# Kernel tuning notes

Measured on AMD Instinct MI355X. Metric: run time of the kernel, lower is better.

The kernel has to match this reference:

```python
import jax, jax.numpy as jnp
import numpy as np

N_HEADS = 16
POOL_WIDTH = 3


def setup_inputs() -> dict:
    key = jax.random.key(0)
    ks = jax.random.split(key, 6)
    B, S, D = 4, 1024, 1024
    x = jax.random.normal(ks[0], (B, S, D), dtype=jnp.float32)
    W_q = jax.random.normal(ks[1], (D, D), dtype=jnp.float32) * 0.02
    W_k = jax.random.normal(ks[2], (D, D), dtype=jnp.float32) * 0.02
    W_v = jax.random.normal(ks[3], (D, D), dtype=jnp.float32) * 0.02
    W_o = jax.random.normal(ks[4], (D, D), dtype=jnp.float32) * 0.02
    freq_raw = jnp.zeros((D,), dtype=jnp.float32)
    pool_raw = jnp.array([0.25, 1.0, 0.25], dtype=jnp.float32)
    return {"x": x, "W_q": W_q, "W_k": W_k, "W_v": W_v, "W_o": W_o,
            "freq_raw": freq_raw, "pool_raw": pool_raw}


def _spectral_attention(x, W_q, W_k, W_v, W_o, freq_raw, pool_raw):
    B, S, D = x.shape
    H = N_HEADS
    hd = D // H
    pw = POOL_WIDTH
    pad = pw // 2

    # projections (torch Linear: y = x @ W.T)
    Q = x @ W_q.T
    K = x @ W_k.T
    V = x @ W_v.T

    # monotone non-increasing freq weights: reverse cumsum of softplus
    fw = jnp.flip(jnp.cumsum(jnp.flip(jax.nn.softplus(freq_raw))))
    # symmetric, positive pool weights
    pwts = jax.nn.softplus((pool_raw + jnp.flip(pool_raw)) * 0.5)

    Qh = (Q * fw).reshape(B, S, H, hd).transpose(0, 2, 1, 3)  # [B,H,S,hd]
    K_pad = jnp.pad(K, ((0, 0), (0, 0), (pad, pad)))          # [B,S,D+2*pad]

    scores = jnp.zeros((B, H, S, S), dtype=x.dtype)
    for i in range(pw):  # small fixed loop over pool offsets
        K_shift = jax.lax.dynamic_slice_in_dim(K_pad, i, D, axis=2)
        Kh = K_shift.reshape(B, S, H, hd).transpose(0, 2, 1, 3)
        scores = scores + pwts[i] * jnp.einsum('bhqd,bhkd->bhqk', Qh, Kh)
    scores = scores / np.sqrt(hd).astype(x.dtype)

    causal = jnp.tril(jnp.ones((S, S), dtype=bool))
    scores = jnp.where(causal, scores, jnp.finfo(scores.dtype).min)
    attn = jax.nn.softmax(scores, axis=-1)

    Vh = V.reshape(B, S, H, hd).transpose(0, 2, 1, 3)
    out = jnp.einsum('bhqk,bhkd->bhqd', attn, Vh)
    out = out.transpose(0, 2, 1, 3).reshape(B, S, D)
    return out @ W_o.T


def reference(x, W_q, W_k, W_v, W_o, freq_raw, pool_raw):
    return _spectral_attention(x, W_q, W_k, W_v, W_o, freq_raw, pool_raw)
```

## Files before the change

kernel.cpp:

```cpp
#include <hip/hip_runtime.h>

typedef __attribute__((ext_vector_type(8))) short short8;
typedef __attribute__((ext_vector_type(4))) float float4v;
typedef __attribute__((ext_vector_type(4))) float floatx4;
typedef __attribute__((ext_vector_type(4))) unsigned short ushort4v;

#define DEV static __device__ __forceinline__
#define MFMA __builtin_amdgcn_mfma_f32_16x16x32_bf16

DEV unsigned short f2bf(float f){
  unsigned u = __builtin_bit_cast(unsigned, f);
  unsigned r = u + 0x7FFFu + ((u >> 16) & 1u);
  return (unsigned short)(r >> 16);
}
DEV float bf2f(unsigned short h){
  unsigned u = ((unsigned)h) << 16;
  return __builtin_bit_cast(float, u);
}
DEV float softplus_f(float x){
  if (x > 20.f) return x;
  return log1pf(expf(x));
}

DEV void gload16(const void* g, void* l){
  __builtin_amdgcn_global_load_lds(
      (const __attribute__((address_space(1))) unsigned int*)g,
      (__attribute__((address_space(3))) unsigned int*)l, 16, 0, 0);
}

__global__ void k_prep_fw(const float* __restrict__ freq_raw,
                          const float* __restrict__ pool_raw,
                          float* __restrict__ fw, float* __restrict__ pw){
  __shared__ float s[1024];
  int d = threadIdx.x;
  s[d] = softplus_f(freq_raw[d]);
  __syncthreads();
  for (int off = 1; off < 1024; off <<= 1){
    float t = (d + off < 1024) ? s[d + off] : 0.f;
    __syncthreads();
    s[d] += t;
    __syncthreads();
  }
  fw[d] = s[d];
  if (d < 3) pw[d] = softplus_f((pool_raw[d] + pool_raw[2 - d]) * 0.5f);
}

__global__ __launch_bounds__(256) void k_prep_w(
    const float* __restrict__ Wq, const float* __restrict__ Wk,
    const float* __restrict__ Wv, const float* __restrict__ Wo,
    const float* __restrict__ fw, const float* __restrict__ pw,
    unsigned short* __restrict__ wq_h, unsigned short* __restrict__ wq_l,
    unsigned short* __restrict__ wk_h, unsigned short* __restrict__ wk_l,
    unsigned short* __restrict__ wv_b, unsigned short* __restrict__ wo_b){
  int idx = blockIdx.x * 256 + threadIdx.x;
  int n  = idx >> 8;
  int k4 = (idx & 255) << 2;
  float p0 = pw[0], p1 = pw[1], p2 = pw[2];
  float f = fw[n] * 0.125f;
  int o = n * 1024 + k4;
  float4v q4 = *(const float4v*)(Wq + o);
  float4v k0v = *(const float4v*)(Wk + o);
  float4v km = {0.f,0.f,0.f,0.f}, kp = {0.f,0.f,0.f,0.f};
  if (n > 0)    km = *(const float4v*)(Wk + o - 1024);
  if (n < 1023) kp = *(const float4v*)(Wk + o + 1024);
  float4v v4 = *(const float4v*)(Wv + o);
  float4v o4 = *(const float4v*)(Wo + o);
  ushort4v qh, ql, kh, kl, vb, ob;
  for (int j = 0; j < 4; j++){
    float wq_ = f * q4[j];
    unsigned short h = f2bf(wq_);
    qh[j] = h; ql[j] = f2bf(wq_ - bf2f(h));
    float wk_ = p0 * km[j] + p1 * k0v[j] + p2 * kp[j];
    h = f2bf(wk_);
    kh[j] = h; kl[j] = f2bf(wk_ - bf2f(h));
    vb[j] = f2bf(v4[j]);
    ob[j] = f2bf(o4[j]);
  }
  *(ushort4v*)(wq_h + o) = qh; *(ushort4v*)(wq_l + o) = ql;
  *(ushort4v*)(wk_h + o) = kh; *(ushort4v*)(wk_l + o) = kl;
  *(ushort4v*)(wv_b + o) = vb; *(ushort4v*)(wo_b + o) = ob;
}

__global__ __launch_bounds__(256) void k_split_x(const float* __restrict__ x,
                                                 unsigned short* __restrict__ xh,
                                                 unsigned short* __restrict__ xl){
  int idx = blockIdx.x * 256 + threadIdx.x;
  int o = idx * 4;
  float4v v = *(const float4v*)(x + o);
  ushort4v h4, l4;
  for (int j = 0; j < 4; j++){
    unsigned short h = f2bf(v[j]);
    h4[j] = h; l4[j] = f2bf(v[j] - bf2f(h));
  }
  *(ushort4v*)(xh + o) = h4;
  *(ushort4v*)(xl + o) = l4;
}

__global__ __launch_bounds__(256) void k_gemm_qk(
    const unsigned short* __restrict__ Ah, const unsigned short* __restrict__ Al,
    const unsigned short* __restrict__ Bqh, const unsigned short* __restrict__ Bql,
    const unsigned short* __restrict__ Bkh, const unsigned short* __restrict__ Bkl,
    unsigned short* __restrict__ qh_o, unsigned short* __restrict__ ql_o,
    unsigned short* __restrict__ kh_o, unsigned short* __restrict__ kl_o){
  __shared__ unsigned short lds[2][16384];
  int tid = threadIdx.x;
  int w = tid >> 6, l = tid & 63, lg = l >> 4, lr = l & 15;
  int wr = w >> 1, wc = w & 1;
  int g = blockIdx.x;
  int mblk = (g & 7) * 4 + ((g >> 3) & 3);
  int nblk = g >> 5;
  int m0 = mblk * 128, n0 = nblk * 64;

  auto stage = [&](int kt, int bufi){
    unsigned short* buf = lds[bufi];
    for (int rep = 0; rep < 2; rep++){
      int idx = rep * 256 + tid;
      int r = idx >> 2, c = idx & 3;
      int cs = (c ^ ((r >> 1) & 3)) * 8;
      int srcA = (m0 + r) * 1024 + kt + cs;
      unsigned short* dst = buf + rep * 2048 + w * 512;
      gload16(Ah + srcA, dst);
      gload16(Al + srcA, dst + 4096);
    }
    {
      int r = tid >> 2, c = tid & 3;
      int cs = (c ^ ((r >> 1) & 3)) * 8;
      int srcB = (n0 + r) * 1024 + kt + cs;
      unsigned short* dst = buf + 8192 + w * 512;
      gload16(Bqh + srcB, dst);
      gload16(Bql + srcB, dst + 2048);
      gload16(Bkh + srcB, dst + 4096);
      gload16(Bkl + srcB, dst + 6144);
    }
  };

  floatx4 aq[4][2] = {}, ak[4][2] = {};
  stage(0, 0);
  __syncthreads();
  int cur = 0;
  for (int kt = 0; kt < 1024; kt += 32){
    if (kt + 32 < 1024) stage(kt + 32, cur ^ 1);
    const unsigned short* buf = lds[cur];
    short8 a_h[4], a_l[4], bq_h[2], bq_l[2], bk_h[2], bk_l[2];
    for (int ms = 0; ms < 4; ms++){
      int r = wr * 64 + ms * 16 + lr;
      int off = r * 32 + ((lg ^ ((r >> 1) & 3)) * 8);
      a_h[ms] = *(const short8*)(buf + off);
      a_l[ms] = *(const short8*)(buf + 4096 + off);
    }
    for (int ns = 0; ns < 2; ns++){
      int r = wc * 32 + ns * 16 + lr;
      int off = r * 32 + ((lg ^ ((r >> 1) & 3)) * 8);
      bq_h[ns] = *(const short8*)(buf + 8192 + off);
      bq_l[ns] = *(const short8*)(buf + 10240 + off);
      bk_h[ns] = *(const short8*)(buf + 12288 + off);
      bk_l[ns] = *(const short8*)(buf + 14336 + off);
    }
    for (int ms = 0; ms < 4; ms++)
      for (int ns = 0; ns < 2; ns++){
        aq[ms][ns] = MFMA(a_h[ms], bq_h[ns], aq[ms][ns], 0, 0, 0);
        aq[ms][ns] = MFMA(a_h[ms], bq_l[ns], aq[ms][ns], 0, 0, 0);
        aq[ms][ns] = MFMA(a_l[ms], bq_h[ns], aq[ms][ns], 0, 0, 0);
        ak[ms][ns] = MFMA(a_h[ms], bk_h[ns], ak[ms][ns], 0, 0, 0);
        ak[ms][ns] = MFMA(a_h[ms], bk_l[ns], ak[ms][ns], 0, 0, 0);
        ak[ms][ns] = MFMA(a_l[ms], bk_h[ns], ak[ms][ns], 0, 0, 0);
      }
    __syncthreads();
    cur ^= 1;
  }
  for (int ms = 0; ms < 4; ms++)
    for (int ns = 0; ns < 2; ns++){
      int mrow = m0 + wr * 64 + ms * 16 + lg * 4;
      int ncol = n0 + wc * 32 + ns * 16 + lr;
      for (int rr = 0; rr < 4; rr++){
        int o = (mrow + rr) * 1024 + ncol;
        float v = aq[ms][ns][rr];
        unsigned short hh = f2bf(v);
        qh_o[o] = hh; ql_o[o] = f2bf(v - bf2f(hh));
        v = ak[ms][ns][rr];
        hh = f2bf(v);
        kh_o[o] = hh; kl_o[o] = f2bf(v - bf2f(hh));
      }
    }
}

template<int OUT>
__global__ __launch_bounds__(256) void k_gemm(
    const unsigned short* __restrict__ Ah, const unsigned short* __restrict__ Bh,
    void* __restrict__ out0, int M, int N, int K){
  constexpr int BUFN = 6144;
  __shared__ unsigned short lds[2 * BUFN];
  int tid = threadIdx.x;
  int w = tid >> 6, l = tid & 63, lg = l >> 4, lr = l & 15;
  int wr = w >> 1, wc = w & 1;
  int n0 = blockIdx.x * 128, m0 = blockIdx.y * 64;

  auto stage = [&](int kt, int bufi){
    unsigned short* buf = lds + bufi * BUFN;
    { int r = tid >> 2, c = tid & 3;
      int src = (m0 + r) * K + kt + (c ^ ((r >> 1) & 3)) * 8;
      gload16(Ah + src, buf + w * 512); }
    for (int rep = 0; rep < 2; rep++){
      int idx = rep * 256 + tid;
      int r = idx >> 2, c = idx & 3;
      int src = (n0 + r) * K + kt + (c ^ ((r >> 1) & 3)) * 8;
      gload16(Bh + src, buf + 2048 + rep * 2048 + w * 512);
    }
  };

  floatx4 acc[2][4] = {};
  stage(0, 0);
  __syncthreads();
  int cur = 0;
  for (int kt = 0; kt < K; kt += 32){
    if (kt + 32 < K) stage(kt + 32, cur ^ 1);
    const unsigned short* buf = lds + cur * BUFN;
    short8 a_h[2], b_h[4];
    for (int ms = 0; ms < 2; ms++){
      int r = wr * 32 + ms * 16 + lr;
      int off = r * 32 + ((lg ^ ((r >> 1) & 3)) * 8);
      a_h[ms] = *(const short8*)(buf + off);
    }
    for (int ns = 0; ns < 4; ns++){
      int r = wc * 64 + ns * 16 + lr;
      int off = r * 32 + ((lg ^ ((r >> 1) & 3)) * 8);
      b_h[ns] = *(const short8*)(buf + 2048 + off);
    }
    for (int ms = 0; ms < 2; ms++)
      for (int ns = 0; ns < 4; ns++)
        acc[ms][ns] = MFMA(a_h[ms], b_h[ns], acc[ms][ns], 0, 0, 0);
    __syncthreads();
    cur ^= 1;
  }
  for (int ms = 0; ms < 2; ms++)
    for (int ns = 0; ns < 4; ns++){
      int mrow = m0 + wr * 32 + ms * 16 + lg * 4;
      int ncol;
      if constexpr (OUT == 3){
        int p = ((ns >> 1) << 5) | ((lr >> 2) << 3) | ((ns & 1) << 2) | (lr & 3);
        ncol = n0 + wc * 64 + p;
      } else {
        ncol = n0 + wc * 64 + ns * 16 + lr;
      }
      for (int rr = 0; rr < 4; rr++){
        float v = acc[ms][ns][rr];
        int o = (mrow + rr) * N + ncol;
        if constexpr (OUT == 2) ((float*)out0)[o] = v;
        else                    ((unsigned short*)out0)[o] = f2bf(v);
      }
    }
}

__global__ __launch_bounds__(256) void k_attn(
    const unsigned short* __restrict__ Qh, const unsigned short* __restrict__ Ql,
    const unsigned short* __restrict__ Kh, const unsigned short* __restrict__ Kl,
    const unsigned short* __restrict__ Vt, unsigned short* __restrict__ Ob){
  __shared__ unsigned short s_k[2][12288];
  int tid = threadIdx.x;
  int w = tid >> 6, l = tid & 63, lg = l >> 4, lr = l & 15;
  int gx = blockIdx.x;
  int bh = gx & 63, qt = gx >> 6;
  int b = bh >> 4, h = bh & 15;
  int q0 = qt * 64;
  int qs = q0 + w * 16;
  int rowb = b * 1024;

  auto stage = [&](int kt, int bufi){
    int k0 = kt * 64;
    unsigned short* buf = s_k[bufi];
    for (int rep = 0; rep < 2; rep++){
      int idx = rep * 256 + tid;
      int r = idx >> 3, c = idx & 7;
      int cs = c ^ (r & 7);
      int srcK = (rowb + k0 + r) * 1024 + h * 64 + cs * 8;
      int srcV = ((h * 64 + r) * 4 + b) * 1024 + k0 + cs * 8;
      unsigned short* dst = buf + rep * 2048 + w * 512;
      gload16(Kh + srcK, dst);
      gload16(Kl + srcK, dst + 4096);
      gload16(Vt + srcV, dst + 8192);
    }
  };

  short8 fqh[2], fql[2];
  for (int ds = 0; ds < 2; ds++){
    int off = (rowb + qs + lr) * 1024 + h * 64 + ds * 32 + lg * 8;
    fqh[ds] = *(const short8*)(Qh + off);
    fql[ds] = *(const short8*)(Ql + off);
  }

  floatx4 oT[4] = {};
  float m_r = -__builtin_inff(), l_r = 0.f;

  int ntile = qt + 1;
  stage(0, 0);
  __syncthreads();
  int cur = 0;
  for (int kt = 0; kt < ntile; kt++){
    int k0 = kt * 64;
    if (kt + 1 < ntile) stage(kt + 1, cur ^ 1);
    const unsigned short* kb = s_k[cur];

    floatx4 sc[4] = {};
    __builtin_amdgcn_s_setprio(1);
    for (int ds = 0; ds < 2; ds++)
      for (int s = 0; s < 4; s++){
        int r = s * 16 + lr;
        int off = r * 64 + (((ds * 4 + lg) ^ (r & 7)) * 8);
        short8 kh_f = *(const short8*)(kb + off);
        short8 kl_f = *(const short8*)(kb + 4096 + off);
        sc[s] = MFMA(kh_f, fqh[ds], sc[s], 0, 0, 0);
        sc[s] = MFMA(kl_f, fqh[ds], sc[s], 0, 0, 0);
        sc[s] = MFMA(kh_f, fql[ds], sc[s], 0, 0, 0);
      }
    __builtin_amdgcn_s_setprio(0);

    if (kt == ntile - 1){
      #pragma unroll
      for (int s = 0; s < 4; s++)
        #pragma unroll
        for (int rr = 0; rr < 4; rr++)
          if (k0 + s * 16 + 4 * lg + rr > qs + lr) sc[s][rr] = -__builtin_inff();
    }

    float mx = sc[0][0];
    #pragma unroll
    for (int s = 0; s < 4; s++)
      #pragma unroll
      for (int rr = 0; rr < 4; rr++) mx = fmaxf(mx, sc[s][rr]);
    mx = fmaxf(mx, __shfl_xor(mx, 16));
    mx = fmaxf(mx, __shfl_xor(mx, 32));
    float mn = fmaxf(m_r, mx);
    float fac = __expf(m_r - mn);
    m_r = mn;
    float ps = 0.f;
    #pragma unroll
    for (int s = 0; s < 4; s++)
      #pragma unroll
      for (int rr = 0; rr < 4; rr++){
        float p = __expf(sc[s][rr] - mn);
        sc[s][rr] = p;
        ps += p;
      }
    ps += __shfl_xor(ps, 16);
    ps += __shfl_xor(ps, 32);
    l_r = l_r * fac + ps;
    #pragma unroll
    for (int dsb = 0; dsb < 4; dsb++) oT[dsb] *= fac;

    __builtin_amdgcn_s_setprio(1);
    #pragma unroll
    for (int kk = 0; kk < 2; kk++){
      short8 pb;
      #pragma unroll
      for (int j = 0; j < 8; j++)
        pb[j] = (short)f2bf(sc[2 * kk + (j >> 2)][j & 3]);
      #pragma unroll
      for (int dsb = 0; dsb < 4; dsb++){
        int rv = dsb * 16 + lr;
        int offv = rv * 64 + (((kk * 4 + lg) ^ (rv & 7)) * 8);
        short8 vb = *(const short8*)(kb + 8192 + offv);
        oT[dsb] = MFMA(vb, pb, oT[dsb], 0, 0, 0);
      }
    }
    __builtin_amdgcn_s_setprio(0);
    __syncthreads();
    cur ^= 1;
  }

  float inv = 1.f / l_r;
  int base = (rowb + qs + lr) * 1024 + h * 64;
  #pragma unroll
  for (int dsb = 0; dsb < 4; dsb++){
    ushort4v o4;
    #pragma unroll
    for (int rr = 0; rr < 4; rr++) o4[rr] = f2bf(oT[dsb][rr] * inv);
    *(ushort4v*)(Ob + base + dsb * 16 + 4 * lg) = o4;
  }
}

extern "C" void kernel_launch(void* const* d_in, const int* in_sizes, int n_in,
                              void* d_out, int out_size, void* d_ws, size_t ws_size,
                              hipStream_t stream){
  const float* x  = (const float*)d_in[0];
  const float* Wq = (const float*)d_in[1];
  const float* Wk = (const float*)d_in[2];
  const float* Wv = (const float*)d_in[3];
  const float* Wo = (const float*)d_in[4];
  const float* fr = (const float*)d_in[5];
  const float* pr = (const float*)d_in[6];

  char* ws = (char*)d_ws;
  size_t off = 0;
  auto alloc = [&](size_t bytes) -> char* {
    char* p = ws + off;
    off += (bytes + 255) & ~(size_t)255;
    return p;
  };
  float* fw = (float*)alloc(1024 * sizeof(float));
  float* pw = (float*)alloc(256);
  const size_t WB = (size_t)1024 * 1024 * 2;
  unsigned short* wq_h = (unsigned short*)alloc(WB);
  unsigned short* wq_l = (unsigned short*)alloc(WB);
  unsigned short* wk_h = (unsigned short*)alloc(WB);
  unsigned short* wk_l = (unsigned short*)alloc(WB);
  unsigned short* wv_b = (unsigned short*)alloc(WB);
  unsigned short* wo_b = (unsigned short*)alloc(WB);
  const size_t XB = (size_t)4096 * 1024 * 2;
  unsigned short* x_h = (unsigned short*)alloc(XB);
  unsigned short* x_l = (unsigned short*)alloc(XB);
  unsigned short* q_h = (unsigned short*)alloc(XB);
  unsigned short* q_l = (unsigned short*)alloc(XB);
  unsigned short* k_h = (unsigned short*)alloc(XB);
  unsigned short* k_l = (unsigned short*)alloc(XB);
  unsigned short* vt  = (unsigned short*)alloc(XB);
  unsigned short* o_b = x_l;

  k_prep_fw<<<1, 1024, 0, stream>>>(fr, pr, fw, pw);
  k_prep_w<<<1024, 256, 0, stream>>>(Wq, Wk, Wv, Wo, fw, pw,
                                     wq_h, wq_l, wk_h, wk_l, wv_b, wo_b);
  k_split_x<<<4096, 256, 0, stream>>>(x, x_h, x_l);

  k_gemm_qk<<<512, 256, 0, stream>>>(x_h, x_l, wq_h, wq_l, wk_h, wk_l,
                                     q_h, q_l, k_h, k_l);
  dim3 ggv(32, 16);
  k_gemm<3><<<ggv, 256, 0, stream>>>(wv_b, x_h, (void*)vt, 1024, 4096, 1024);
  k_attn<<<1024, 256, 0, stream>>>(q_h, q_l, k_h, k_l, vt, o_b);
  dim3 ggo(8, 64);
  k_gemm<2><<<ggo, 256, 0, stream>>>(o_b, wo_b, d_out, 4096, 1024, 1024);
}
```

Baseline: 144.8 us.

## Triple-buffer GEMM pipelines with vmcnt waits and widen QK GEMM to 512 threads

Both GEMM kernels move from double to triple buffering in LDS, prefetching two k-tiles ahead. A partial s_waitcnt vmcnt followed by a single s_barrier per iteration replaces the two __syncthreads calls. The QK projection kernel now runs 512 threads (8 waves), each wave owning a 64x16 tile, and the MFMA order is regrouped so independent accumulators interleave. This aims to hide global load latency and raise MFMA occupancy, at the cost of more LDS per block and reliance on exact vmcnt counting of async loads.

```diff
diff --git a/kernel.cpp b/kernel.cpp
--- a/kernel.cpp
+++ b/kernel.cpp
@@ -96,92 +96,99 @@
   *(ushort4v*)(xl + o) = l4;
 }
 
-__global__ __launch_bounds__(256) void k_gemm_qk(
+__global__ __launch_bounds__(512) void k_gemm_qk(
     const unsigned short* __restrict__ Ah, const unsigned short* __restrict__ Al,
     const unsigned short* __restrict__ Bqh, const unsigned short* __restrict__ Bql,
     const unsigned short* __restrict__ Bkh, const unsigned short* __restrict__ Bkl,
     unsigned short* __restrict__ qh_o, unsigned short* __restrict__ ql_o,
     unsigned short* __restrict__ kh_o, unsigned short* __restrict__ kl_o){
-  __shared__ unsigned short lds[2][16384];
+  __shared__ unsigned short lds[3][16384];
   int tid = threadIdx.x;
   int w = tid >> 6, l = tid & 63, lg = l >> 4, lr = l & 15;
-  int wr = w >> 1, wc = w & 1;
+  int wr = w >> 2, wc = w & 3;
   int g = blockIdx.x;
   int mblk = (g & 7) * 4 + ((g >> 3) & 3);
   int nblk = g >> 5;
   int m0 = mblk * 128, n0 = nblk * 64;
 
+  const unsigned short* Bp0 = (w < 4) ? Bqh : Bql;
+  const unsigned short* Bp1 = (w < 4) ? Bkh : Bkl;
+
   auto stage = [&](int kt, int bufi){
     unsigned short* buf = lds[bufi];
-    for (int rep = 0; rep < 2; rep++){
-      int idx = rep * 256 + tid;
-      int r = idx >> 2, c = idx & 3;
-      int cs = (c ^ ((r >> 1) & 3)) * 8;
-      int srcA = (m0 + r) * 1024 + kt + cs;
-      unsigned short* dst = buf + rep * 2048 + w * 512;
-      gload16(Ah + srcA, dst);
-      gload16(Al + srcA, dst + 4096);
-    }
     {
       int r = tid >> 2, c = tid & 3;
       int cs = (c ^ ((r >> 1) & 3)) * 8;
+      int srcA = (m0 + r) * 1024 + kt + cs;
+      gload16(Ah + srcA, buf + w * 512);
+      gload16(Al + srcA, buf + 4096 + w * 512);
+    }
+    {
+      int within = tid & 255;
+      int r = within >> 2, c = within & 3;
+      int cs = (c ^ ((r >> 1) & 3)) * 8;
       int srcB = (n0 + r) * 1024 + kt + cs;
-      unsigned short* dst = buf + 8192 + w * 512;
-      gload16(Bqh + srcB, dst);
-      gload16(Bql + srcB, dst + 2048);
-      gload16(Bkh + srcB, dst + 4096);
-      gload16(Bkl + srcB, dst + 6144);
+      gload16(Bp0 + srcB, buf + 8192 + w * 512);
+      gload16(Bp1 + srcB, buf + 12288 + w * 512);
     }
   };
 
-  floatx4 aq[4][2] = {}, ak[4][2] = {};
+  floatx4 aq[4] = {}, ak[4] = {};
   stage(0, 0);
-  __syncthreads();
-  int cur = 0;
-  for (int kt = 0; kt < 1024; kt += 32){
-    if (kt + 32 < 1024) stage(kt + 32, cur ^ 1);
-    const unsigned short* buf = lds[cur];
-    short8 a_h[4], a_l[4], bq_h[2], bq_l[2], bk_h[2], bk_l[2];
+  stage(32, 1);
+  for (int t = 0; t < 32; ++t){
+    if (t == 31) asm volatile("s_waitcnt vmcnt(0)" ::: "memory");
+    else         asm volatile("s_waitcnt vmcnt(4)" ::: "memory");
+    __builtin_amdgcn_sched_barrier(0);
+    __builtin_amdgcn_s_barrier();
+    __builtin_amdgcn_sched_barrier(0);
+    if (t + 2 < 32) stage((t + 2) * 32, (t + 2) % 3);
+
+    const unsigned short* buf = lds[t % 3];
+    short8 a_h[4], a_l[4];
+    #pragma unroll
     for (int ms = 0; ms < 4; ms++){
       int r = wr * 64 + ms * 16 + lr;
       int off = r * 32 + ((lg ^ ((r >> 1) & 3)) * 8);
       a_h[ms] = *(const short8*)(buf + off);
       a_l[ms] = *(const short8*)(buf + 4096 + off);
     }
-    for (int ns = 0; ns < 2; ns++){
-      int r = wc * 32 + ns * 16 + lr;
-      int off = r * 32 + ((lg ^ ((r >> 1) & 3)) * 8);
-      bq_h[ns] = *(const short8*)(buf + 8192 + off);
-      bq_l[ns] = *(const short8*)(buf + 10240 + off);
-      bk_h[ns] = *(const short8*)(buf + 12288 + off);
-      bk_l[ns] = *(const short8*)(buf + 14336 + off);
-    }
-    for (int ms = 0; ms < 4; ms++)
-      for (int ns = 0; ns < 2; ns++){
-        aq[ms][ns] = MFMA(a_h[ms], bq_h[ns], aq[ms][ns], 0, 0, 0);
-        aq[ms][ns] = MFMA(a_h[ms], bq_l[ns], aq[ms][ns], 0, 0, 0);
-        aq[ms][ns] = MFMA(a_l[ms], bq_h[ns], aq[ms][ns], 0, 0, 0);
-        ak[ms][ns] = MFMA(a_h[ms], bk_h[ns], ak[ms][ns], 0, 0, 0);
-        ak[ms][ns] = MFMA(a_h[ms], bk_l[ns], ak[ms][ns], 0, 0, 0);
-        ak[ms][ns] = MFMA(a_l[ms], bk_h[ns], ak[ms][ns], 0, 0, 0);
-      }
-    __syncthreads();
-    cur ^= 1;
-  }
-  for (int ms = 0; ms < 4; ms++)
-    for (int ns = 0; ns < 2; ns++){
-      int mrow = m0 + wr * 64 + ms * 16 + lg * 4;
-      int ncol = n0 + wc * 32 + ns * 16 + lr;
-      for (int rr = 0; rr < 4; rr++){
-        int o = (mrow + rr) * 1024 + ncol;
-        float v = aq[ms][ns][rr];
-        unsigned short hh = f2bf(v);
-        qh_o[o] = hh; ql_o[o] = f2bf(v - bf2f(hh));
-        v = ak[ms][ns][rr];
-        hh = f2bf(v);
-        kh_o[o] = hh; kl_o[o] = f2bf(v - bf2f(hh));
-      }
-    }
+    int rb = wc * 16 + lr;
+    int offb = rb * 32 + ((lg ^ ((rb >> 1) & 3)) * 8);
+    short8 bq_h = *(const short8*)(buf + 8192 + offb);
+    short8 bq_l = *(const short8*)(buf + 10240 + offb);
+    short8 bk_h = *(const short8*)(buf + 12288 + offb);
+    short8 bk_l = *(const short8*)(buf + 14336 + offb);
+    #pragma unroll
+    for (int ms = 0; ms < 4; ms++){
+      aq[ms] = MFMA(a_h[ms], bq_h, aq[ms], 0, 0, 0);
+      ak[ms] = MFMA(a_h[ms], bk_h, ak[ms], 0, 0, 0);
+    }
+    #pragma unroll
+    for (int ms = 0; ms < 4; ms++){
+      aq[ms] = MFMA(a_h[ms], bq_l, aq[ms], 0, 0, 0);
+      ak[ms] = MFMA(a_h[ms], bk_l, ak[ms], 0, 0, 0);
+    }
+    #pragma unroll
+    for (int ms = 0; ms < 4; ms++){
+      aq[ms] = MFMA(a_l[ms], bq_h, aq[ms], 0, 0, 0);
+      ak[ms] = MFMA(a_l[ms], bk_h, ak[ms], 0, 0, 0);
+    }
+  }
+
+  for (int ms = 0; ms < 4; ms++){
+    int mrow = m0 + wr * 64 + ms * 16 + lg * 4;
+    int ncol = n0 + wc * 16 + lr;
+    for (int rr = 0; rr < 4; rr++){
+      int o = (mrow + rr) * 1024 + ncol;
+      float v = aq[ms][rr];
+      unsigned short hh = f2bf(v);
+      qh_o[o] = hh; ql_o[o] = f2bf(v - bf2f(hh));
+      v = ak[ms][rr];
+      hh = f2bf(v);
+      kh_o[o] = hh; kl_o[o] = f2bf(v - bf2f(hh));
+    }
+  }
 }
 
 template<int OUT>
@@ -189,7 +196,7 @@
     const unsigned short* __restrict__ Ah, const unsigned short* __restrict__ Bh,
     void* __restrict__ out0, int M, int N, int K){
   constexpr int BUFN = 6144;
-  __shared__ unsigned short lds[2 * BUFN];
+  __shared__ unsigned short lds[3 * BUFN];
   int tid = threadIdx.x;
   int w = tid >> 6, l = tid & 63, lg = l >> 4, lr = l & 15;
   int wr = w >> 1, wc = w & 1;
@@ -209,28 +216,36 @@
   };
 
   floatx4 acc[2][4] = {};
+  int nT = K >> 5;
   stage(0, 0);
-  __syncthreads();
-  int cur = 0;
-  for (int kt = 0; kt < K; kt += 32){
-    if (kt + 32 < K) stage(kt + 32, cur ^ 1);
-    const unsigned short* buf = lds + cur * BUFN;
+  stage(32, 1);
+  for (int t = 0; t < nT; ++t){
+    if (t == nT - 1) asm volatile("s_waitcnt vmcnt(0)" ::: "memory");
+    else             asm volatile("s_waitcnt vmcnt(3)" ::: "memory");
+    __builtin_amdgcn_sched_barrier(0);
+    __builtin_amdgcn_s_barrier();
+    __builtin_amdgcn_sched_barrier(0);
+    if (t + 2 < nT) stage((t + 2) * 32, (t + 2) % 3);
+
+    const unsigned short* buf = lds + (t % 3) * BUFN;
     short8 a_h[2], b_h[4];
+    #pragma unroll
     for (int ms = 0; ms < 2; ms++){
       int r = wr * 32 + ms * 16 + lr;
       int off = r * 32 + ((lg ^ ((r >> 1) & 3)) * 8);
       a_h[ms] = *(const short8*)(buf + off);
     }
+    #pragma unroll
     for (int ns = 0; ns < 4; ns++){
       int r = wc * 64 + ns * 16 + lr;
       int off = r * 32 + ((lg ^ ((r >> 1) & 3)) * 8);
       b_h[ns] = *(const short8*)(buf + 2048 + off);
     }
+    #pragma unroll
     for (int ms = 0; ms < 2; ms++)
+      #pragma unroll
       for (int ns = 0; ns < 4; ns++)
         acc[ms][ns] = MFMA(a_h[ms], b_h[ns], acc[ms][ns], 0, 0, 0);
-    __syncthreads();
-    cur ^= 1;
   }
   for (int ms = 0; ms < 2; ms++)
     for (int ns = 0; ns < 4; ns++){
@@ -420,7 +435,7 @@
                                      wq_h, wq_l, wk_h, wk_l, wv_b, wo_b);
   k_split_x<<<4096, 256, 0, stream>>>(x, x_h, x_l);
 
-  k_gemm_qk<<<512, 256, 0, stream>>>(x_h, x_l, wq_h, wq_l, wk_h, wk_l,
+  k_gemm_qk<<<512, 512, 0, stream>>>(x_h, x_l, wq_h, wq_l, wk_h, wk_l,
                                      q_h, q_l, k_h, k_l);
   dim3 ggv(32, 16);
   k_gemm<3><<<ggv, 256, 0, stream>>>(wv_b, x_h, (void*)vt, 1024, 4096, 1024);
```

Result: no change. 142.9 us (-1.3%).

## Merge QK and V projection GEMMs into one launch; triple-buffer generic GEMM

Applied to the files above, without the earlier changes.

Combines the split-precision Q/K projection and the V^T projection into a single kernel that picks its role from the block index, interleaving the two kinds of blocks. The goal is to remove a launch and the tail bubble between them so both GEMMs share the GPU. The V and output GEMMs also move to a three-stage LDS ring with explicit vmcnt waits and raw barriers, giving deeper prefetch and one barrier per k-step. The cost is more LDS per block (the merged kernel reserves the larger QK footprint for every block), which can lower occupancy, and uneven work between the two block kinds.

```diff
diff --git a/kernel.cpp b/kernel.cpp
--- a/kernel.cpp
+++ b/kernel.cpp
@@ -96,23 +96,22 @@
   *(ushort4v*)(xl + o) = l4;
 }
 
-__global__ __launch_bounds__(256) void k_gemm_qk(
+
+DEV void qk_body(int sub, unsigned short* lds,
     const unsigned short* __restrict__ Ah, const unsigned short* __restrict__ Al,
     const unsigned short* __restrict__ Bqh, const unsigned short* __restrict__ Bql,
     const unsigned short* __restrict__ Bkh, const unsigned short* __restrict__ Bkl,
     unsigned short* __restrict__ qh_o, unsigned short* __restrict__ ql_o,
     unsigned short* __restrict__ kh_o, unsigned short* __restrict__ kl_o){
-  __shared__ unsigned short lds[2][16384];
   int tid = threadIdx.x;
   int w = tid >> 6, l = tid & 63, lg = l >> 4, lr = l & 15;
   int wr = w >> 1, wc = w & 1;
-  int g = blockIdx.x;
-  int mblk = (g & 7) * 4 + ((g >> 3) & 3);
-  int nblk = g >> 5;
+  int mblk = (sub & 7) * 4 + ((sub >> 3) & 3);
+  int nblk = sub >> 5;
   int m0 = mblk * 128, n0 = nblk * 64;
 
   auto stage = [&](int kt, int bufi){
-    unsigned short* buf = lds[bufi];
+    unsigned short* buf = lds + bufi * 16384;
     for (int rep = 0; rep < 2; rep++){
       int idx = rep * 256 + tid;
       int r = idx >> 2, c = idx & 3;
@@ -140,14 +139,16 @@
   int cur = 0;
   for (int kt = 0; kt < 1024; kt += 32){
     if (kt + 32 < 1024) stage(kt + 32, cur ^ 1);
-    const unsigned short* buf = lds[cur];
+    const unsigned short* buf = lds + cur * 16384;
     short8 a_h[4], a_l[4], bq_h[2], bq_l[2], bk_h[2], bk_l[2];
+    #pragma unroll
     for (int ms = 0; ms < 4; ms++){
       int r = wr * 64 + ms * 16 + lr;
       int off = r * 32 + ((lg ^ ((r >> 1) & 3)) * 8);
       a_h[ms] = *(const short8*)(buf + off);
       a_l[ms] = *(const short8*)(buf + 4096 + off);
     }
+    #pragma unroll
     for (int ns = 0; ns < 2; ns++){
       int r = wc * 32 + ns * 16 + lr;
       int off = r * 32 + ((lg ^ ((r >> 1) & 3)) * 8);
@@ -156,7 +157,9 @@
       bk_h[ns] = *(const short8*)(buf + 12288 + off);
       bk_l[ns] = *(const short8*)(buf + 14336 + off);
     }
+    #pragma unroll
     for (int ms = 0; ms < 4; ms++)
+      #pragma unroll
       for (int ns = 0; ns < 2; ns++){
         aq[ms][ns] = MFMA(a_h[ms], bq_h[ns], aq[ms][ns], 0, 0, 0);
         aq[ms][ns] = MFMA(a_h[ms], bq_l[ns], aq[ms][ns], 0, 0, 0);
@@ -184,16 +187,16 @@
     }
 }
 
-template<int OUT>
-__global__ __launch_bounds__(256) void k_gemm(
+DEV void vt_body(int sub, unsigned short* lds,
     const unsigned short* __restrict__ Ah, const unsigned short* __restrict__ Bh,
-    void* __restrict__ out0, int M, int N, int K){
+    unsigned short* __restrict__ out0){
   constexpr int BUFN = 6144;
-  __shared__ unsigned short lds[2 * BUFN];
+  const int M = 1024, N = 4096, K = 1024;
   int tid = threadIdx.x;
   int w = tid >> 6, l = tid & 63, lg = l >> 4, lr = l & 15;
   int wr = w >> 1, wc = w & 1;
-  int n0 = blockIdx.x * 128, m0 = blockIdx.y * 64;
+  int n0 = (sub & 31) * 128, m0 = (sub >> 5) * 64;
+  (void)M;
 
   auto stage = [&](int kt, int bufi){
     unsigned short* buf = lds + bufi * BUFN;
@@ -209,39 +212,126 @@
   };
 
   floatx4 acc[2][4] = {};
+  int nT = K >> 5;
   stage(0, 0);
-  __syncthreads();
-  int cur = 0;
-  for (int kt = 0; kt < K; kt += 32){
-    if (kt + 32 < K) stage(kt + 32, cur ^ 1);
-    const unsigned short* buf = lds + cur * BUFN;
+  stage(32, 1);
+  for (int t = 0; t < nT; ++t){
+    if (t == nT - 1) asm volatile("s_waitcnt vmcnt(0)" ::: "memory");
+    else             asm volatile("s_waitcnt vmcnt(3)" ::: "memory");
+    __builtin_amdgcn_sched_barrier(0);
+    __builtin_amdgcn_s_barrier();
+    __builtin_amdgcn_sched_barrier(0);
+    if (t + 2 < nT) stage((t + 2) * 32, (t + 2) % 3);
+
+    const unsigned short* buf = lds + (t % 3) * BUFN;
     short8 a_h[2], b_h[4];
+    #pragma unroll
     for (int ms = 0; ms < 2; ms++){
       int r = wr * 32 + ms * 16 + lr;
       int off = r * 32 + ((lg ^ ((r >> 1) & 3)) * 8);
       a_h[ms] = *(const short8*)(buf + off);
     }
+    #pragma unroll
     for (int ns = 0; ns < 4; ns++){
       int r = wc * 64 + ns * 16 + lr;
       int off = r * 32 + ((lg ^ ((r >> 1) & 3)) * 8);
       b_h[ns] = *(const short8*)(buf + 2048 + off);
     }
+    #pragma unroll
     for (int ms = 0; ms < 2; ms++)
+      #pragma unroll
       for (int ns = 0; ns < 4; ns++)
         acc[ms][ns] = MFMA(a_h[ms], b_h[ns], acc[ms][ns], 0, 0, 0);
-    __syncthreads();
-    cur ^= 1;
   }
   for (int ms = 0; ms < 2; ms++)
     for (int ns = 0; ns < 4; ns++){
       int mrow = m0 + wr * 32 + ms * 16 + lg * 4;
-      int ncol;
-      if constexpr (OUT == 3){
-        int p = ((ns >> 1) << 5) | ((lr >> 2) << 3) | ((ns & 1) << 2) | (lr & 3);
-        ncol = n0 + wc * 64 + p;
-      } else {
-        ncol = n0 + wc * 64 + ns * 16 + lr;
-      }
+      int p = ((ns >> 1) << 5) | ((lr >> 2) << 3) | ((ns & 1) << 2) | (lr & 3);
+      int ncol = n0 + wc * 64 + p;
+      for (int rr = 0; rr < 4; rr++){
+        float v = acc[ms][ns][rr];
+        out0[(mrow + rr) * N + ncol] = f2bf(v);
+      }
+    }
+}
+
+__global__ __launch_bounds__(256) void k_qkv(
+    const unsigned short* __restrict__ Ah, const unsigned short* __restrict__ Al,
+    const unsigned short* __restrict__ Bqh, const unsigned short* __restrict__ Bql,
+    const unsigned short* __restrict__ Bkh, const unsigned short* __restrict__ Bkl,
+    unsigned short* __restrict__ qh_o, unsigned short* __restrict__ ql_o,
+    unsigned short* __restrict__ kh_o, unsigned short* __restrict__ kl_o,
+    const unsigned short* __restrict__ Wv, unsigned short* __restrict__ vt_o){
+  __shared__ unsigned short lds[32768];
+  int g = blockIdx.x;
+  int kind = (g >> 3) & 1;
+  int sub = ((g >> 4) << 3) | (g & 7);
+  if (kind == 0)
+    qk_body(sub, lds, Ah, Al, Bqh, Bql, Bkh, Bkl, qh_o, ql_o, kh_o, kl_o);
+  else
+    vt_body(sub, lds, Wv, Ah, vt_o);
+}
+
+template<int OUT>
+__global__ __launch_bounds__(256) void k_gemm(
+    const unsigned short* __restrict__ Ah, const unsigned short* __restrict__ Bh,
+    void* __restrict__ out0, int M, int N, int K){
+  constexpr int BUFN = 6144;
+  __shared__ unsigned short lds[3 * BUFN];
+  int tid = threadIdx.x;
+  int w = tid >> 6, l = tid & 63, lg = l >> 4, lr = l & 15;
+  int wr = w >> 1, wc = w & 1;
+  int n0 = blockIdx.x * 128, m0 = blockIdx.y * 64;
+
+  auto stage = [&](int kt, int bufi){
+    unsigned short* buf = lds + bufi * BUFN;
+    { int r = tid >> 2, c = tid & 3;
+      int src = (m0 + r) * K + kt + (c ^ ((r >> 1) & 3)) * 8;
+      gload16(Ah + src, buf + w * 512); }
+    for (int rep = 0; rep < 2; rep++){
+      int idx = rep * 256 + tid;
+      int r = idx >> 2, c = idx & 3;
+      int src = (n0 + r) * K + kt + (c ^ ((r >> 1) & 3)) * 8;
+      gload16(Bh + src, buf + 2048 + rep * 2048 + w * 512);
+    }
+  };
+
+  floatx4 acc[2][4] = {};
+  int nT = K >> 5;
+  stage(0, 0);
+  stage(32, 1);
+  for (int t = 0; t < nT; ++t){
+    if (t == nT - 1) asm volatile("s_waitcnt vmcnt(0)" ::: "memory");
+    else             asm volatile("s_waitcnt vmcnt(3)" ::: "memory");
+    __builtin_amdgcn_sched_barrier(0);
+    __builtin_amdgcn_s_barrier();
+    __builtin_amdgcn_sched_barrier(0);
+    if (t + 2 < nT) stage((t + 2) * 32, (t + 2) % 3);
+
+    const unsigned short* buf = lds + (t % 3) * BUFN;
+    short8 a_h[2], b_h[4];
+    #pragma unroll
+    for (int ms = 0; ms < 2; ms++){
+      int r = wr * 32 + ms * 16 + lr;
+      int off = r * 32 + ((lg ^ ((r >> 1) & 3)) * 8);
+      a_h[ms] = *(const short8*)(buf + off);
+    }
+    #pragma unroll
+    for (int ns = 0; ns < 4; ns++){
+      int r = wc * 64 + ns * 16 + lr;
+      int off = r * 32 + ((lg ^ ((r >> 1) & 3)) * 8);
+      b_h[ns] = *(const short8*)(buf + 2048 + off);
+    }
+    #pragma unroll
+    for (int ms = 0; ms < 2; ms++)
+      #pragma unroll
+      for (int ns = 0; ns < 4; ns++)
+        acc[ms][ns] = MFMA(a_h[ms], b_h[ns], acc[ms][ns], 0, 0, 0);
+  }
+  for (int ms = 0; ms < 2; ms++)
+    for (int ns = 0; ns < 4; ns++){
+      int mrow = m0 + wr * 32 + ms * 16 + lg * 4;
+      int ncol = n0 + wc * 64 + ns * 16 + lr;
       for (int rr = 0; rr < 4; rr++){
         float v = acc[ms][ns][rr];
         int o = (mrow + rr) * N + ncol;
@@ -420,10 +510,8 @@
                                      wq_h, wq_l, wk_h, wk_l, wv_b, wo_b);
   k_split_x<<<4096, 256, 0, stream>>>(x, x_h, x_l);
 
-  k_gemm_qk<<<512, 256, 0, stream>>>(x_h, x_l, wq_h, wq_l, wk_h, wk_l,
-                                     q_h, q_l, k_h, k_l);
-  dim3 ggv(32, 16);
-  k_gemm<3><<<ggv, 256, 0, stream>>>(wv_b, x_h, (void*)vt, 1024, 4096, 1024);
+  k_qkv<<<1024, 256, 0, stream>>>(x_h, x_l, wq_h, wq_l, wk_h, wk_l,
+                                  q_h, q_l, k_h, k_l, wv_b, vt);
   k_attn<<<1024, 256, 0, stream>>>(q_h, q_l, k_h, k_l, vt, o_b);
   dim3 ggo(8, 64);
   k_gemm<2><<<ggo, 256, 0, stream>>>(o_b, wo_b, d_out, 4096, 1024, 1024);
```

Result: slower. 151.2 us (+4.4%).

## Fuse V projection into QK GEMM and triple-buffer output GEMM

Applied to the files above, without the earlier changes.

Moves the V projection into the Q/K projection kernel, so the staged x tiles are reused for a seventh MFMA stream and the transposed V is written straight from its accumulators. This drops a separate GEMM launch and a second pass over x. The generic GEMM, now used only for the output projection, switches to a three-stage LDS pipeline with explicit vmcnt waits and a single barrier per iteration. The cost is more LDS and accumulator registers in the fused kernel, which may lower occupancy, plus a scattered store layout for vt.

```diff
diff --git a/kernel.cpp b/kernel.cpp
--- a/kernel.cpp
+++ b/kernel.cpp
@@ -96,13 +96,15 @@
   *(ushort4v*)(xl + o) = l4;
 }
 
-__global__ __launch_bounds__(256) void k_gemm_qk(
+__global__ __launch_bounds__(256) void k_qkv(
     const unsigned short* __restrict__ Ah, const unsigned short* __restrict__ Al,
     const unsigned short* __restrict__ Bqh, const unsigned short* __restrict__ Bql,
     const unsigned short* __restrict__ Bkh, const unsigned short* __restrict__ Bkl,
+    const unsigned short* __restrict__ Bvh,
     unsigned short* __restrict__ qh_o, unsigned short* __restrict__ ql_o,
-    unsigned short* __restrict__ kh_o, unsigned short* __restrict__ kl_o){
-  __shared__ unsigned short lds[2][16384];
+    unsigned short* __restrict__ kh_o, unsigned short* __restrict__ kl_o,
+    unsigned short* __restrict__ vt_o){
+  __shared__ unsigned short lds[2][18432];
   int tid = threadIdx.x;
   int w = tid >> 6, l = tid & 63, lg = l >> 4, lr = l & 15;
   int wr = w >> 1, wc = w & 1;
@@ -131,23 +133,26 @@
       gload16(Bql + srcB, dst + 2048);
       gload16(Bkh + srcB, dst + 4096);
       gload16(Bkl + srcB, dst + 6144);
+      gload16(Bvh + srcB, dst + 8192);
     }
   };
 
-  floatx4 aq[4][2] = {}, ak[4][2] = {};
+  floatx4 aq[4][2] = {}, ak[4][2] = {}, av[4][2] = {};
   stage(0, 0);
   __syncthreads();
   int cur = 0;
   for (int kt = 0; kt < 1024; kt += 32){
     if (kt + 32 < 1024) stage(kt + 32, cur ^ 1);
     const unsigned short* buf = lds[cur];
-    short8 a_h[4], a_l[4], bq_h[2], bq_l[2], bk_h[2], bk_l[2];
+    short8 a_h[4], a_l[4], bq_h[2], bq_l[2], bk_h[2], bk_l[2], bv_h[2];
+    #pragma unroll
     for (int ms = 0; ms < 4; ms++){
       int r = wr * 64 + ms * 16 + lr;
       int off = r * 32 + ((lg ^ ((r >> 1) & 3)) * 8);
       a_h[ms] = *(const short8*)(buf + off);
       a_l[ms] = *(const short8*)(buf + 4096 + off);
     }
+    #pragma unroll
     for (int ns = 0; ns < 2; ns++){
       int r = wc * 32 + ns * 16 + lr;
       int off = r * 32 + ((lg ^ ((r >> 1) & 3)) * 8);
@@ -155,8 +160,11 @@
       bq_l[ns] = *(const short8*)(buf + 10240 + off);
       bk_h[ns] = *(const short8*)(buf + 12288 + off);
       bk_l[ns] = *(const short8*)(buf + 14336 + off);
-    }
+      bv_h[ns] = *(const short8*)(buf + 16384 + off);
+    }
+    #pragma unroll
     for (int ms = 0; ms < 4; ms++)
+      #pragma unroll
       for (int ns = 0; ns < 2; ns++){
         aq[ms][ns] = MFMA(a_h[ms], bq_h[ns], aq[ms][ns], 0, 0, 0);
         aq[ms][ns] = MFMA(a_h[ms], bq_l[ns], aq[ms][ns], 0, 0, 0);
@@ -164,6 +172,7 @@
         ak[ms][ns] = MFMA(a_h[ms], bk_h[ns], ak[ms][ns], 0, 0, 0);
         ak[ms][ns] = MFMA(a_h[ms], bk_l[ns], ak[ms][ns], 0, 0, 0);
         ak[ms][ns] = MFMA(a_l[ms], bk_h[ns], ak[ms][ns], 0, 0, 0);
+        av[ms][ns] = MFMA(a_h[ms], bv_h[ns], av[ms][ns], 0, 0, 0);
       }
     __syncthreads();
     cur ^= 1;
@@ -181,6 +190,12 @@
         hh = f2bf(v);
         kh_o[o] = hh; kl_o[o] = f2bf(v - bf2f(hh));
       }
+      int tb = m0 + wr * 64;
+      int bq = tb >> 10, sg = (tb >> 6) & 15;
+      int P0 = ((ms >> 1) << 5) | (lg << 3) | ((ms & 1) << 2);
+      ushort4v v4;
+      for (int rr = 0; rr < 4; rr++) v4[rr] = f2bf(av[ms][ns][rr]);
+      *(ushort4v*)(vt_o + (ncol * 4 + bq) * 1024 + sg * 64 + P0) = v4;
     }
 }
 
@@ -189,7 +204,7 @@
     const unsigned short* __restrict__ Ah, const unsigned short* __restrict__ Bh,
     void* __restrict__ out0, int M, int N, int K){
   constexpr int BUFN = 6144;
-  __shared__ unsigned short lds[2 * BUFN];
+  __shared__ unsigned short lds[3 * BUFN];
   int tid = threadIdx.x;
   int w = tid >> 6, l = tid & 63, lg = l >> 4, lr = l & 15;
   int wr = w >> 1, wc = w & 1;
@@ -209,39 +224,41 @@
   };
 
   floatx4 acc[2][4] = {};
+  int nT = K >> 5;
   stage(0, 0);
-  __syncthreads();
-  int cur = 0;
-  for (int kt = 0; kt < K; kt += 32){
-    if (kt + 32 < K) stage(kt + 32, cur ^ 1);
-    const unsigned short* buf = lds + cur * BUFN;
+  stage(32, 1);
+  for (int t = 0; t < nT; ++t){
+    if (t == nT - 1) asm volatile("s_waitcnt vmcnt(0)" ::: "memory");
+    else             asm volatile("s_waitcnt vmcnt(3)" ::: "memory");
+    __builtin_amdgcn_sched_barrier(0);
+    __builtin_amdgcn_s_barrier();
+    __builtin_amdgcn_sched_barrier(0);
+    if (t + 2 < nT) stage((t + 2) * 32, (t + 2) % 3);
+
+    const unsigned short* buf = lds + (t % 3) * BUFN;
     short8 a_h[2], b_h[4];
+    #pragma unroll
     for (int ms = 0; ms < 2; ms++){
       int r = wr * 32 + ms * 16 + lr;
       int off = r * 32 + ((lg ^ ((r >> 1) & 3)) * 8);
       a_h[ms] = *(const short8*)(buf + off);
     }
+    #pragma unroll
     for (int ns = 0; ns < 4; ns++){
       int r = wc * 64 + ns * 16 + lr;
       int off = r * 32 + ((lg ^ ((r >> 1) & 3)) * 8);
       b_h[ns] = *(const short8*)(buf + 2048 + off);
     }
+    #pragma unroll
     for (int ms = 0; ms < 2; ms++)
+      #pragma unroll
       for (int ns = 0; ns < 4; ns++)
         acc[ms][ns] = MFMA(a_h[ms], b_h[ns], acc[ms][ns], 0, 0, 0);
-    __syncthreads();
-    cur ^= 1;
   }
   for (int ms = 0; ms < 2; ms++)
     for (int ns = 0; ns < 4; ns++){
       int mrow = m0 + wr * 32 + ms * 16 + lg * 4;
-      int ncol;
-      if constexpr (OUT == 3){
-        int p = ((ns >> 1) << 5) | ((lr >> 2) << 3) | ((ns & 1) << 2) | (lr & 3);
-        ncol = n0 + wc * 64 + p;
-      } else {
-        ncol = n0 + wc * 64 + ns * 16 + lr;
-      }
+      int ncol = n0 + wc * 64 + ns * 16 + lr;
       for (int rr = 0; rr < 4; rr++){
         float v = acc[ms][ns][rr];
         int o = (mrow + rr) * N + ncol;
@@ -420,10 +437,8 @@
                                      wq_h, wq_l, wk_h, wk_l, wv_b, wo_b);
   k_split_x<<<4096, 256, 0, stream>>>(x, x_h, x_l);
 
-  k_gemm_qk<<<512, 256, 0, stream>>>(x_h, x_l, wq_h, wq_l, wk_h, wk_l,
-                                     q_h, q_l, k_h, k_l);
-  dim3 ggv(32, 16);
-  k_gemm<3><<<ggv, 256, 0, stream>>>(wv_b, x_h, (void*)vt, 1024, 4096, 1024);
+  k_qkv<<<512, 256, 0, stream>>>(x_h, x_l, wq_h, wq_l, wk_h, wk_l, wv_b,
+                                 q_h, q_l, k_h, k_l, vt);
   k_attn<<<1024, 256, 0, stream>>>(q_h, q_l, k_h, k_l, vt, o_b);
   dim3 ggo(8, 64);
   k_gemm<2><<<ggo, 256, 0, stream>>>(o_b, wo_b, d_out, 4096, 1024, 1024);
```

Measured after the change: 132.4 us. -8.6%, faster.
